# Kernel tuning notes

Measured on AMD Instinct MI355X. Metric: run time of the kernel, lower is better.

Reference implementation:

```python
import jax, jax.numpy as jnp
import numpy as np

N_NODES = 50000
N_EDGES = 800000
D_FEAT = 128
UNITS = 128


def setup_inputs() -> dict:
    key = jax.random.key(0)
    k1, k2, k3, k4, k5 = jax.random.split(key, 5)
    node_states = jax.random.normal(k1, (N_NODES, D_FEAT), dtype=jnp.float32)
    src = jnp.sort(jax.random.randint(k2, (N_EDGES,), 0, N_NODES))
    dst = jax.random.randint(k3, (N_EDGES,), 0, N_NODES)
    edges = jnp.stack([src, dst], axis=1).astype(jnp.int64)  # [E,2], sorted by source
    kernel = jax.random.normal(k4, (D_FEAT, UNITS), dtype=jnp.float32) * (1.0 / np.sqrt(D_FEAT))
    kernel_attention = jax.random.normal(k5, (2 * UNITS, 1), dtype=jnp.float32) * (1.0 / np.sqrt(2 * UNITS))
    return {"node_states": node_states, "edges": edges, "kernel": kernel, "kernel_attention": kernel_attention}


def reference(node_states, edges, kernel, kernel_attention):
    n_nodes = node_states.shape[0]
    src, dst = edges[:, 0], edges[:, 1]
    # linear transform of node features
    h = node_states @ kernel                                  # [N, U]
    # per-edge concatenated (src, dst) features -> raw attention logit
    e_feat = jnp.concatenate([h[src], h[dst]], axis=-1)       # [E, 2U]
    logits = jax.nn.leaky_relu((e_feat @ kernel_attention)[:, 0], negative_slope=0.2)  # [E]
    scores = jnp.exp(jnp.clip(logits, -2.0, 2.0))             # [E]
    # segment softmax over incoming edges of each source node
    denom = jax.ops.segment_sum(scores, src, num_segments=n_nodes)  # [N]
    alpha = scores / denom[src]                                # [E]
    # weighted aggregation of neighbor features
    out = jax.ops.segment_sum(h[dst] * alpha[:, None], src, num_segments=n_nodes)  # [N, U]
    return out
```

## Files before the change

### kernel.cpp

```cpp
#include <hip/hip_runtime.h>

#define N_NODES 50000
#define N_EDGES 800000
#define D 128
#define LDA 136

#define SEARCH_BLOCKS 196
#define GEMM_BLOCKS   391

typedef __attribute__((ext_vector_type(8))) short bf16x8;
typedef __attribute__((ext_vector_type(4))) float f32x4;

__device__ __forceinline__ unsigned short f2bf(float f) {
    union { float f; unsigned u; } v; v.f = f;
    return (unsigned short)((v.u + 0x7fffu + ((v.u >> 16) & 1u)) >> 16);
}
__device__ __forceinline__ float bflo(unsigned u) {
    union { unsigned u; float f; } c; c.u = u << 16; return c.f;
}
__device__ __forceinline__ float bfhi(unsigned u) {
    union { unsigned u; float f; } c; c.u = u & 0xffff0000u; return c.f;
}

__global__ __launch_bounds__(256) void kh_fused(const float* __restrict__ X,
                                                const int* __restrict__ edges,
                                                const float* __restrict__ W,
                                                const float* __restrict__ ka,
                                                unsigned short* __restrict__ h,
                                                float* __restrict__ a_src,
                                                float* __restrict__ a_dst,
                                                int* __restrict__ row_ptr) {
    __shared__ unsigned short As[128 * LDA];
    __shared__ unsigned short Bs[128 * LDA];
    __shared__ float kas[2 * D];
    int b = blockIdx.x, tid = threadIdx.x;

    if (b < SEARCH_BLOCKS) {
        int n = b * 256 + tid;
        if (n > N_NODES) return;
        int lo = 0, hi = N_EDGES;
        while (lo < hi) {
            int mid = (lo + hi) >> 1;
            if (edges[2 * mid] < n) lo = mid + 1; else hi = mid;
        }
        row_ptr[n] = lo;
        return;
    }

    int row0 = (b - SEARCH_BLOCKS) * 128;
    kas[tid] = ka[tid];
    for (int i = tid; i < 128 * 32; i += 256) {
        int k = i >> 5, n4 = (i & 31) * 4;
        float4 w = *(const float4*)(W + k * D + n4);
        Bs[(n4 + 0) * LDA + k] = f2bf(w.x);
        Bs[(n4 + 1) * LDA + k] = f2bf(w.y);
        Bs[(n4 + 2) * LDA + k] = f2bf(w.z);
        Bs[(n4 + 3) * LDA + k] = f2bf(w.w);
    }
    for (int i = tid; i < 2048; i += 256) {
        int r = i >> 4, c = i & 15;
        int gr = row0 + r;
        union { unsigned short us[8]; uint4 q; } pk;
        if (gr < N_NODES) {
            const float* xp = X + (size_t)gr * D + c * 8;
#pragma unroll
            for (int j = 0; j < 8; ++j) pk.us[j] = f2bf(xp[j]);
        } else pk.q = make_uint4(0u, 0u, 0u, 0u);
        *(uint4*)&As[r * LDA + c * 8] = pk.q;
    }
    __syncthreads();

    int wave = tid >> 6, lane = tid & 63;
    int m16 = lane & 15, quad = lane >> 4;
    int wr0 = wave * 32;
    f32x4 acc[2][8];
#pragma unroll
    for (int i = 0; i < 2; ++i)
#pragma unroll
        for (int j = 0; j < 8; ++j) acc[i][j] = (f32x4){0.f, 0.f, 0.f, 0.f};

    for (int k0 = 0; k0 < D; k0 += 32) {
        bf16x8 a0 = *(const bf16x8*)&As[(wr0 + m16) * LDA + k0 + quad * 8];
        bf16x8 a1 = *(const bf16x8*)&As[(wr0 + 16 + m16) * LDA + k0 + quad * 8];
#pragma unroll
        for (int j = 0; j < 8; ++j) {
            bf16x8 bf = *(const bf16x8*)&Bs[(j * 16 + m16) * LDA + k0 + quad * 8];
            acc[0][j] = __builtin_amdgcn_mfma_f32_16x16x32_bf16(a0, bf, acc[0][j], 0, 0, 0);
            acc[1][j] = __builtin_amdgcn_mfma_f32_16x16x32_bf16(a1, bf, acc[1][j], 0, 0, 0);
        }
    }

#pragma unroll
    for (int i = 0; i < 2; ++i)
#pragma unroll
        for (int j = 0; j < 8; ++j)
#pragma unroll
            for (int r = 0; r < 4; ++r) {
                int row = row0 + wr0 + i * 16 + quad * 4 + r;
                if (row < N_NODES)
                    h[(size_t)row * D + j * 16 + m16] = f2bf(acc[i][j][r]);
            }

#pragma unroll
    for (int i = 0; i < 2; ++i)
#pragma unroll
        for (int r = 0; r < 4; ++r) {
            float ps = 0.f, pd = 0.f;
#pragma unroll
            for (int j = 0; j < 8; ++j) {
                float val = acc[i][j][r];
                ps += val * kas[j * 16 + m16];
                pd += val * kas[D + j * 16 + m16];
            }
            for (int off = 8; off > 0; off >>= 1) {
                ps += __shfl_down(ps, off, 16);
                pd += __shfl_down(pd, off, 16);
            }
            int row = row0 + wr0 + i * 16 + quad * 4 + r;
            if (m16 == 0 && row < N_NODES) { a_src[row] = ps; a_dst[row] = pd; }
        }
}

__global__ __launch_bounds__(256) void k3(const int* __restrict__ edges,
                                          const int* __restrict__ row_ptr,
                                          const unsigned short* __restrict__ h,
                                          const float* __restrict__ a_src,
                                          const float* __restrict__ a_dst,
                                          float* __restrict__ out) {
    int node = blockIdx.x * 4 + (threadIdx.x >> 6);
    if (node >= N_NODES) return;
    int lane = threadIdx.x & 63;
    int q = lane >> 4;
    int l16 = lane & 15;

    int start = row_ptr[node], end = row_ptr[node + 1];
    float asn = a_src[node];

    float4 accA = make_float4(0.f, 0.f, 0.f, 0.f);
    float4 accB = make_float4(0.f, 0.f, 0.f, 0.f);
    float dn = 0.f;

    for (int base = start; base < end; base += 64) {
        int cnt = min(64, end - base);
        int d = 0; float s = 0.f;
        if (lane < cnt) {
            d = edges[2 * (base + lane) + 1];
            float lg = asn + a_dst[d];
            lg = (lg >= 0.f) ? lg : 0.2f * lg;
            lg = fminf(fmaxf(lg, -2.f), 2.f);
            s = __expf(lg);
        }
        for (int j = 0; j < cnt; j += 16) {
            float sj[4]; int dj[4];
#pragma unroll
            for (int t = 0; t < 4; ++t) {
                sj[t] = __shfl(s, j + q + 4 * t, 64);
                dj[t] = __shfl(d, j + q + 4 * t, 64);
            }
            uint4 p[4];
#pragma unroll
            for (int t = 0; t < 4; ++t)
                p[t] = *(const uint4*)(h + ((size_t)dj[t] << 7) + (l16 << 3));
#pragma unroll
            for (int t = 0; t < 4; ++t) {
                float sv = sj[t];
                accA.x += sv * bflo(p[t].x); accA.y += sv * bfhi(p[t].x);
                accA.z += sv * bflo(p[t].y); accA.w += sv * bfhi(p[t].y);
                accB.x += sv * bflo(p[t].z); accB.y += sv * bfhi(p[t].z);
                accB.z += sv * bflo(p[t].w); accB.w += sv * bfhi(p[t].w);
                dn += sv;
            }
        }
    }

    float vals[9] = {accA.x, accA.y, accA.z, accA.w,
                     accB.x, accB.y, accB.z, accB.w, dn};
#pragma unroll
    for (int m = 32; m >= 16; m >>= 1)
#pragma unroll
        for (int i = 0; i < 9; ++i) vals[i] += __shfl_xor(vals[i], m, 64);

    if (q == 0) {
        float inv = (end > start) ? 1.f / vals[8] : 0.f;
        float4 o0 = make_float4(vals[0] * inv, vals[1] * inv, vals[2] * inv, vals[3] * inv);
        float4 o1 = make_float4(vals[4] * inv, vals[5] * inv, vals[6] * inv, vals[7] * inv);
        float* op = out + (size_t)node * D + l16 * 8;
        *(float4*)op = o0;
        *(float4*)(op + 4) = o1;
    }
}

extern "C" void kernel_launch(void* const* d_in, const int* in_sizes, int n_in,
                              void* d_out, int out_size, void* d_ws, size_t ws_size,
                              hipStream_t stream) {
    const float* X     = (const float*)d_in[0];
    const int*   edges = (const int*)d_in[1];
    const float* W     = (const float*)d_in[2];
    const float* ka    = (const float*)d_in[3];

    char* ws = (char*)d_ws;
    unsigned short* h  = (unsigned short*)ws;
    float* a_src   = (float*)(ws + (size_t)N_NODES * D * 2);
    float* a_dst   = a_src + N_NODES;
    int*   row_ptr = (int*)(a_dst + N_NODES);
    float* out = (float*)d_out;

    kh_fused<<<SEARCH_BLOCKS + GEMM_BLOCKS, 256, 0, stream>>>(
        X, edges, W, ka, h, a_src, a_dst, row_ptr);
    k3<<<(N_NODES + 3) / 4, 256, 0, stream>>>(edges, row_ptr, h, a_src, a_dst, out);
}
```

Before: 126.8 us.

## Load GEMM A directly from global, compact dst indices, map node per 16 lanes

The GEMM stage drops the LDS staging of X and loads fp32 rows straight into registers with nontemporal loads, converting to bf16 in place before the MFMAs. The search blocks also copy the destination column of the int64 edge list into a compact int32 array, which halves the index traffic in the aggregation kernel. The aggregation kernel now gives each node 16 lanes instead of a 64-lane wave, with 8 gathers in flight per step and no cross-lane reduction, and writes the output with nontemporal stores. The trade-off is lower memory-level parallelism per node and possible load imbalance across skewed degrees, in exchange for less wasted work on low-degree nodes.

```diff
diff --git a/kernel.cpp b/kernel.cpp
--- a/kernel.cpp
+++ b/kernel.cpp
@@ -29,21 +29,24 @@
                                                 unsigned short* __restrict__ h,
                                                 float* __restrict__ a_src,
                                                 float* __restrict__ a_dst,
-                                                int* __restrict__ row_ptr) {
-    __shared__ unsigned short As[128 * LDA];
+                                                int* __restrict__ row_ptr,
+                                                int* __restrict__ dst32) {
     __shared__ unsigned short Bs[128 * LDA];
     __shared__ float kas[2 * D];
     int b = blockIdx.x, tid = threadIdx.x;
 
     if (b < SEARCH_BLOCKS) {
         int n = b * 256 + tid;
-        if (n > N_NODES) return;
-        int lo = 0, hi = N_EDGES;
-        while (lo < hi) {
-            int mid = (lo + hi) >> 1;
-            if (edges[2 * mid] < n) lo = mid + 1; else hi = mid;
-        }
-        row_ptr[n] = lo;
+        if (n <= N_NODES) {
+            int lo = 0, hi = N_EDGES;
+            while (lo < hi) {
+                int mid = (lo + hi) >> 1;
+                if (edges[2 * mid] < n) lo = mid + 1; else hi = mid;
+            }
+            row_ptr[n] = lo;
+        }
+        for (int e = b * 256 + tid; e < N_EDGES; e += SEARCH_BLOCKS * 256)
+            dst32[e] = edges[2 * e + 1];
         return;
     }
 
@@ -57,36 +60,38 @@
         Bs[(n4 + 2) * LDA + k] = f2bf(w.z);
         Bs[(n4 + 3) * LDA + k] = f2bf(w.w);
     }
-    for (int i = tid; i < 2048; i += 256) {
-        int r = i >> 4, c = i & 15;
-        int gr = row0 + r;
-        union { unsigned short us[8]; uint4 q; } pk;
-        if (gr < N_NODES) {
-            const float* xp = X + (size_t)gr * D + c * 8;
-#pragma unroll
-            for (int j = 0; j < 8; ++j) pk.us[j] = f2bf(xp[j]);
-        } else pk.q = make_uint4(0u, 0u, 0u, 0u);
-        *(uint4*)&As[r * LDA + c * 8] = pk.q;
-    }
     __syncthreads();
 
     int wave = tid >> 6, lane = tid & 63;
     int m16 = lane & 15, quad = lane >> 4;
     int wr0 = wave * 32;
+    int gr0 = min(row0 + wr0 + m16, N_NODES - 1);
+    int gr1 = min(row0 + wr0 + 16 + m16, N_NODES - 1);
+    const float* x0 = X + (size_t)gr0 * D + quad * 8;
+    const float* x1 = X + (size_t)gr1 * D + quad * 8;
+
     f32x4 acc[2][8];
 #pragma unroll
     for (int i = 0; i < 2; ++i)
 #pragma unroll
         for (int j = 0; j < 8; ++j) acc[i][j] = (f32x4){0.f, 0.f, 0.f, 0.f};
 
+#pragma unroll
     for (int k0 = 0; k0 < D; k0 += 32) {
-        bf16x8 a0 = *(const bf16x8*)&As[(wr0 + m16) * LDA + k0 + quad * 8];
-        bf16x8 a1 = *(const bf16x8*)&As[(wr0 + 16 + m16) * LDA + k0 + quad * 8];
+        f32x4 f00 = __builtin_nontemporal_load((const f32x4*)(x0 + k0));
+        f32x4 f01 = __builtin_nontemporal_load((const f32x4*)(x0 + k0 + 4));
+        f32x4 f10 = __builtin_nontemporal_load((const f32x4*)(x1 + k0));
+        f32x4 f11 = __builtin_nontemporal_load((const f32x4*)(x1 + k0 + 4));
+        union { unsigned short us[8]; bf16x8 v; } ua0, ua1;
+#pragma unroll
+        for (int j = 0; j < 4; ++j) { ua0.us[j] = f2bf(f00[j]); ua0.us[4 + j] = f2bf(f01[j]); }
+#pragma unroll
+        for (int j = 0; j < 4; ++j) { ua1.us[j] = f2bf(f10[j]); ua1.us[4 + j] = f2bf(f11[j]); }
 #pragma unroll
         for (int j = 0; j < 8; ++j) {
             bf16x8 bf = *(const bf16x8*)&Bs[(j * 16 + m16) * LDA + k0 + quad * 8];
-            acc[0][j] = __builtin_amdgcn_mfma_f32_16x16x32_bf16(a0, bf, acc[0][j], 0, 0, 0);
-            acc[1][j] = __builtin_amdgcn_mfma_f32_16x16x32_bf16(a1, bf, acc[1][j], 0, 0, 0);
+            acc[0][j] = __builtin_amdgcn_mfma_f32_16x16x32_bf16(ua0.v, bf, acc[0][j], 0, 0, 0);
+            acc[1][j] = __builtin_amdgcn_mfma_f32_16x16x32_bf16(ua1.v, bf, acc[1][j], 0, 0, 0);
         }
     }
 
@@ -121,73 +126,60 @@
         }
 }
 
-__global__ __launch_bounds__(256) void k3(const int* __restrict__ edges,
+__global__ __launch_bounds__(256) void k3(const int* __restrict__ dst32,
                                           const int* __restrict__ row_ptr,
                                           const unsigned short* __restrict__ h,
                                           const float* __restrict__ a_src,
                                           const float* __restrict__ a_dst,
                                           float* __restrict__ out) {
-    int node = blockIdx.x * 4 + (threadIdx.x >> 6);
-    if (node >= N_NODES) return;
-    int lane = threadIdx.x & 63;
-    int q = lane >> 4;
-    int l16 = lane & 15;
+    int node = blockIdx.x * 16 + (threadIdx.x >> 4);
+    int l16 = threadIdx.x & 15;
 
     int start = row_ptr[node], end = row_ptr[node + 1];
     float asn = a_src[node];
-
-    float4 accA = make_float4(0.f, 0.f, 0.f, 0.f);
-    float4 accB = make_float4(0.f, 0.f, 0.f, 0.f);
+    const unsigned short* hl = h + (l16 << 3);
+
+    float accv[8] = {0.f, 0.f, 0.f, 0.f, 0.f, 0.f, 0.f, 0.f};
     float dn = 0.f;
 
-    for (int base = start; base < end; base += 64) {
-        int cnt = min(64, end - base);
-        int d = 0; float s = 0.f;
-        if (lane < cnt) {
-            d = edges[2 * (base + lane) + 1];
-            float lg = asn + a_dst[d];
+    for (int base = start; base < end; base += 16) {
+        int cnt = min(16, end - base);
+        int dd = 0; float s = 0.f;
+        if (l16 < cnt) {
+            dd = dst32[base + l16];
+            float lg = asn + a_dst[dd];
             lg = (lg >= 0.f) ? lg : 0.2f * lg;
             lg = fminf(fmaxf(lg, -2.f), 2.f);
             s = __expf(lg);
         }
-        for (int j = 0; j < cnt; j += 16) {
-            float sj[4]; int dj[4];
-#pragma unroll
-            for (int t = 0; t < 4; ++t) {
-                sj[t] = __shfl(s, j + q + 4 * t, 64);
-                dj[t] = __shfl(d, j + q + 4 * t, 64);
-            }
-            uint4 p[4];
-#pragma unroll
-            for (int t = 0; t < 4; ++t)
-                p[t] = *(const uint4*)(h + ((size_t)dj[t] << 7) + (l16 << 3));
-#pragma unroll
-            for (int t = 0; t < 4; ++t) {
+        for (int t0 = 0; t0 < cnt; t0 += 8) {
+            float sj[8]; int dj[8]; uint4 p[8];
+#pragma unroll
+            for (int t = 0; t < 8; ++t) {
+                sj[t] = __shfl(s, t0 + t, 16);
+                dj[t] = __shfl(dd, t0 + t, 16);
+            }
+#pragma unroll
+            for (int t = 0; t < 8; ++t)
+                p[t] = *(const uint4*)(hl + ((size_t)dj[t] << 7));
+#pragma unroll
+            for (int t = 0; t < 8; ++t) {
                 float sv = sj[t];
-                accA.x += sv * bflo(p[t].x); accA.y += sv * bfhi(p[t].x);
-                accA.z += sv * bflo(p[t].y); accA.w += sv * bfhi(p[t].y);
-                accB.x += sv * bflo(p[t].z); accB.y += sv * bfhi(p[t].z);
-                accB.z += sv * bflo(p[t].w); accB.w += sv * bfhi(p[t].w);
+                accv[0] += sv * bflo(p[t].x); accv[1] += sv * bfhi(p[t].x);
+                accv[2] += sv * bflo(p[t].y); accv[3] += sv * bfhi(p[t].y);
+                accv[4] += sv * bflo(p[t].z); accv[5] += sv * bfhi(p[t].z);
+                accv[6] += sv * bflo(p[t].w); accv[7] += sv * bfhi(p[t].w);
                 dn += sv;
             }
         }
     }
 
-    float vals[9] = {accA.x, accA.y, accA.z, accA.w,
-                     accB.x, accB.y, accB.z, accB.w, dn};
-#pragma unroll
-    for (int m = 32; m >= 16; m >>= 1)
-#pragma unroll
-        for (int i = 0; i < 9; ++i) vals[i] += __shfl_xor(vals[i], m, 64);
-
-    if (q == 0) {
-        float inv = (end > start) ? 1.f / vals[8] : 0.f;
-        float4 o0 = make_float4(vals[0] * inv, vals[1] * inv, vals[2] * inv, vals[3] * inv);
-        float4 o1 = make_float4(vals[4] * inv, vals[5] * inv, vals[6] * inv, vals[7] * inv);
-        float* op = out + (size_t)node * D + l16 * 8;
-        *(float4*)op = o0;
-        *(float4*)(op + 4) = o1;
-    }
+    float inv = (end > start) ? 1.f / dn : 0.f;
+    f32x4 o0 = {accv[0] * inv, accv[1] * inv, accv[2] * inv, accv[3] * inv};
+    f32x4 o1 = {accv[4] * inv, accv[5] * inv, accv[6] * inv, accv[7] * inv};
+    float* op = out + (size_t)node * D + l16 * 8;
+    __builtin_nontemporal_store(o0, (f32x4*)op);
+    __builtin_nontemporal_store(o1, (f32x4*)(op + 4));
 }
 
 extern "C" void kernel_launch(void* const* d_in, const int* in_sizes, int n_in,
@@ -203,9 +195,10 @@
     float* a_src   = (float*)(ws + (size_t)N_NODES * D * 2);
     float* a_dst   = a_src + N_NODES;
     int*   row_ptr = (int*)(a_dst + N_NODES);
+    int*   dst32   = row_ptr + ((N_NODES + 16) & ~15);
     float* out = (float*)d_out;
 
     kh_fused<<<SEARCH_BLOCKS + GEMM_BLOCKS, 256, 0, stream>>>(
-        X, edges, W, ka, h, a_src, a_dst, row_ptr);
-    k3<<<(N_NODES + 3) / 4, 256, 0, stream>>>(edges, row_ptr, h, a_src, a_dst, out);
-}
+        X, edges, W, ka, h, a_src, a_dst, row_ptr, dst32);
+    k3<<<(N_NODES + 15) / 16, 256, 0, stream>>>(dst32, row_ptr, h, a_src, a_dst, out);
+}
```

Result: slower. 137.3 us (+8.3%).

## Precompute edge scores in separate kernel, vectorize X loads, nontemporal output stores

Applied to the files above, without the earlier changes.

Adds a flat per-edge kernel that computes the attention scores into a workspace buffer, so the aggregation kernel only loads a precomputed score instead of gathering a_dst and evaluating exp. The GEMM staging now loads X with float4 vector loads instead of scalar loads, and the output is written with nontemporal stores. The new kernel costs an extra launch plus roughly 10 MB of added edge and score traffic, in exchange for taking the dependent a_dst gather out of the aggregation loop's critical path.

```diff
diff --git a/kernel.cpp b/kernel.cpp
--- a/kernel.cpp
+++ b/kernel.cpp
@@ -63,8 +63,12 @@
         union { unsigned short us[8]; uint4 q; } pk;
         if (gr < N_NODES) {
             const float* xp = X + (size_t)gr * D + c * 8;
-#pragma unroll
-            for (int j = 0; j < 8; ++j) pk.us[j] = f2bf(xp[j]);
+            float4 u = *(const float4*)xp;
+            float4 v = *(const float4*)(xp + 4);
+            pk.us[0] = f2bf(u.x); pk.us[1] = f2bf(u.y);
+            pk.us[2] = f2bf(u.z); pk.us[3] = f2bf(u.w);
+            pk.us[4] = f2bf(v.x); pk.us[5] = f2bf(v.y);
+            pk.us[6] = f2bf(v.z); pk.us[7] = f2bf(v.w);
         } else pk.q = make_uint4(0u, 0u, 0u, 0u);
         *(uint4*)&As[r * LDA + c * 8] = pk.q;
     }
@@ -121,11 +125,23 @@
         }
 }
 
+__global__ __launch_bounds__(256) void k2_scores(const int* __restrict__ edges,
+                                                 const float* __restrict__ a_src,
+                                                 const float* __restrict__ a_dst,
+                                                 float* __restrict__ scores) {
+    int e = blockIdx.x * 256 + threadIdx.x;
+    if (e >= N_EDGES) return;
+    int2 sd = ((const int2*)edges)[e];
+    float lg = a_src[sd.x] + a_dst[sd.y];
+    lg = (lg >= 0.f) ? lg : 0.2f * lg;
+    lg = fminf(fmaxf(lg, -2.f), 2.f);
+    scores[e] = __expf(lg);
+}
+
 __global__ __launch_bounds__(256) void k3(const int* __restrict__ edges,
                                           const int* __restrict__ row_ptr,
+                                          const float* __restrict__ scores,
                                           const unsigned short* __restrict__ h,
-                                          const float* __restrict__ a_src,
-                                          const float* __restrict__ a_dst,
                                           float* __restrict__ out) {
     int node = blockIdx.x * 4 + (threadIdx.x >> 6);
     if (node >= N_NODES) return;
@@ -134,7 +150,6 @@
     int l16 = lane & 15;
 
     int start = row_ptr[node], end = row_ptr[node + 1];
-    float asn = a_src[node];
 
     float4 accA = make_float4(0.f, 0.f, 0.f, 0.f);
     float4 accB = make_float4(0.f, 0.f, 0.f, 0.f);
@@ -145,10 +160,7 @@
         int d = 0; float s = 0.f;
         if (lane < cnt) {
             d = edges[2 * (base + lane) + 1];
-            float lg = asn + a_dst[d];
-            lg = (lg >= 0.f) ? lg : 0.2f * lg;
-            lg = fminf(fmaxf(lg, -2.f), 2.f);
-            s = __expf(lg);
+            s = scores[base + lane];
         }
         for (int j = 0; j < cnt; j += 16) {
             float sj[4]; int dj[4];
@@ -182,11 +194,11 @@
 
     if (q == 0) {
         float inv = (end > start) ? 1.f / vals[8] : 0.f;
-        float4 o0 = make_float4(vals[0] * inv, vals[1] * inv, vals[2] * inv, vals[3] * inv);
-        float4 o1 = make_float4(vals[4] * inv, vals[5] * inv, vals[6] * inv, vals[7] * inv);
+        f32x4 o0 = {vals[0] * inv, vals[1] * inv, vals[2] * inv, vals[3] * inv};
+        f32x4 o1 = {vals[4] * inv, vals[5] * inv, vals[6] * inv, vals[7] * inv};
         float* op = out + (size_t)node * D + l16 * 8;
-        *(float4*)op = o0;
-        *(float4*)(op + 4) = o1;
+        __builtin_nontemporal_store(o0, (f32x4*)op);
+        __builtin_nontemporal_store(o1, (f32x4*)(op + 4));
     }
 }
 
@@ -203,9 +215,11 @@
     float* a_src   = (float*)(ws + (size_t)N_NODES * D * 2);
     float* a_dst   = a_src + N_NODES;
     int*   row_ptr = (int*)(a_dst + N_NODES);
+    float* scores  = (float*)(row_ptr + ((N_NODES + 16) & ~15));
     float* out = (float*)d_out;
 
     kh_fused<<<SEARCH_BLOCKS + GEMM_BLOCKS, 256, 0, stream>>>(
         X, edges, W, ka, h, a_src, a_dst, row_ptr);
-    k3<<<(N_NODES + 3) / 4, 256, 0, stream>>>(edges, row_ptr, h, a_src, a_dst, out);
-}
+    k2_scores<<<(N_EDGES + 255) / 256, 256, 0, stream>>>(edges, a_src, a_dst, scores);
+    k3<<<(N_NODES + 3) / 4, 256, 0, stream>>>(edges, row_ptr, scores, h, out);
+}
```

Measured after the change: 129.6 us. 2.3% more time.
